# Optimization experiments

Hardware: AMD Instinct MI355X
Metric: run time of the kernel (lower is better)

## Reference

```python
import jax, jax.numpy as jnp
import numpy as np

K = 16
RADIUS = 1.0
N = 16384
SEQ = 8


def _knn(pc, k):
    """Brute-force kNN of pc against itself. pc: (1, n, 3).
    Returns (dist, idx) each (1, n, k), sorted ascending by distance,
    matching pointutils.knn semantics (Euclidean distance)."""
    x2 = jnp.sum(pc * pc, axis=-1)  # (1, n)
    # d2[b,i,j] = ||p_i - p_j||^2 via expansion; avoids (n,n,3) intermediate
    d2 = x2[:, :, None] + x2[:, None, :] - 2.0 * jnp.einsum('bnd,bmd->bnm', pc, pc)
    d2 = jnp.maximum(d2, 0.0)
    neg_d2, idx = jax.lax.top_k(-d2, k)  # k smallest distances
    dist = jnp.sqrt(jnp.maximum(-neg_d2, 0.0))
    return dist, idx


def setup_inputs() -> dict:
    key = jax.random.key(0)
    k1, k2, k3 = jax.random.split(key, 3)
    return {
        'pc_source': jax.random.normal(k1, (1, N, 3), dtype=jnp.float32),
        'pred_flow': jax.random.normal(k2, (SEQ, N, 3), dtype=jnp.float32),
        'weights': jax.random.uniform(k3, (N,), dtype=jnp.float32),
    }


def reference(pc_source, pred_flow, weights):
    # flow: (seq, 3, n)
    flow = jnp.transpose(pred_flow, (0, 2, 1))
    dist, idx = _knn(pc_source, K)  # (1, n, k)
    # replace out-of-radius neighbors with the nearest (self) index
    idx = jnp.where(dist > RADIUS, idx[:, :, 0:1], idx)
    idx = idx[0]  # (n, k); identical for all sequence steps
    # grouping_operation: gather neighbor flows -> (seq, 3, n, k)
    nn_flow = flow[:, :, idx]
    diff = flow[:, :, :, None] - nn_flow  # (seq, 3, n, k)
    # L2 norm over channel dim (loss_norm=2), safe at 0 (self-neighbor)
    sq = jnp.sum(diff * diff, axis=1)  # (seq, n, k)
    norm = jnp.where(sq > 0, jnp.sqrt(jnp.where(sq > 0, sq, 1.0)), 0.0)
    loss = norm.mean(axis=-1)  # (seq, n)
    loss = loss * weights[None, :]
    loss = loss.sum(axis=1)  # (seq,)
    wsum = weights.sum()
    loss = jnp.where(wsum > 0, loss / wsum, loss)
    return loss.mean()
```

## Files before the change

### kernel.cpp

```cpp
#include <hip/hip_runtime.h>
#include <math.h>

#define NPTS  16384
#define KNN   16
#define SEQV  8
#define NW    16
#define BATCH 8
#define CAPM  15
#define CAPR  1.001f
#define NBKT  256
#define BSCALE 56.8888f
#define HBLK  16
#define NGRP  256

#define SLOT(arr, t, col) arr[(t) * 1024 + (col)]

#define WS_HIST   256
#define WS_STARTS 16640
#define WS_SIDX   17920
#define WS_SORTED 83488

__device__ __forceinline__ unsigned umin_(unsigned a, unsigned b) { return a < b ? a : b; }
__device__ __forceinline__ unsigned umax_(unsigned a, unsigned b) { return a > b ? a : b; }

__device__ __forceinline__ int nbucket(float x) { return (int)fminf(x * BSCALE, 255.0f); }

__device__ __forceinline__ void merge_one(unsigned keys[KNN], unsigned kk) {
    if (kk < keys[KNN - 1]) {
#pragma unroll
        for (int u = 0; u < KNN; ++u) {
            unsigned lo = umin_(kk, keys[u]);
            kk = umax_(kk, keys[u]);
            keys[u] = lo;
        }
    }
}

__device__ __forceinline__ void merge16(unsigned k[KNN], const unsigned o[KNN]) {
    unsigned v[KNN];
#pragma unroll
    for (int i = 0; i < KNN; ++i) v[i] = umin_(k[i], o[KNN - 1 - i]);
#pragma unroll
    for (int d = 8; d >= 1; d >>= 1) {
#pragma unroll
        for (int i = 0; i < KNN; ++i) {
            if ((i & d) == 0) {
                unsigned lo = umin_(v[i], v[i + d]);
                unsigned hi = umax_(v[i], v[i + d]);
                v[i] = lo; v[i + d] = hi;
            }
        }
    }
#pragma unroll
    for (int i = 0; i < KNN; ++i) k[i] = v[i];
}

__device__ __forceinline__ void tree_load_merge(unsigned* uS, unsigned keys[KNN], int src) {
    unsigned o[KNN];
#pragma unroll
    for (int t = 0; t < KNN; ++t) o[t] = SLOT(uS, t, src);
    merge16(keys, o);
}

__global__ __launch_bounds__(1024) void hist_kernel(
    const float* __restrict__ pc, unsigned* __restrict__ hist)
{
    __shared__ unsigned h[NBKT];
    const int tid = threadIdx.x;
    if (tid < NBKT) h[tid] = 0u;
    __syncthreads();
    const int i = blockIdx.x * 1024 + tid;
    const float x = pc[3 * i + 0], y = pc[3 * i + 1], z = pc[3 * i + 2];
    const float n = sqrtf(fmaf(x, x, fmaf(y, y, z * z)));
    atomicAdd(&h[nbucket(n)], 1u);
    __syncthreads();
    if (tid < NBKT) hist[tid * HBLK + blockIdx.x] = h[tid];
}

__global__ __launch_bounds__(1024) void scatter_kernel(
    const float* __restrict__ pc, const unsigned* __restrict__ hist,
    unsigned* __restrict__ starts, float* __restrict__ accum,
    unsigned* __restrict__ sidx, float4* __restrict__ sorted4)
{
    __shared__ unsigned sH[NBKT];
    __shared__ unsigned sBase[NBKT];
    __shared__ unsigned sCnt[NBKT];
    const int tid = threadIdx.x;
    const int b   = blockIdx.x;

    unsigned own = 0, pre = 0;
    if (tid < NBKT) {
        const unsigned* row = hist + tid * HBLK;
        unsigned s = 0, p = 0;
#pragma unroll
        for (int k = 0; k < HBLK; ++k) {
            const unsigned c = row[k];
            if (k < b) p += c;
            s += c;
        }
        own = s; pre = p;
        sH[tid] = s;
        sCnt[tid] = 0u;
    }
    __syncthreads();
    for (int off = 1; off < NBKT; off <<= 1) {
        unsigned a = 0u;
        if (tid < NBKT && tid >= off) a = sH[tid - off];
        __syncthreads();
        if (tid < NBKT) sH[tid] += a;
        __syncthreads();
    }
    if (tid < NBKT) {
        const unsigned excl = sH[tid] - own;
        sBase[tid] = excl + pre;
        if (b == 0) starts[tid] = excl;
    }
    if (b == 0 && tid == 0) starts[NBKT] = NPTS;
    if (b == 0 && tid < 8) ((unsigned*)accum)[tid] = 0u;
    __syncthreads();

    const int i = b * 1024 + tid;
    const float x = pc[3 * i + 0], y = pc[3 * i + 1], z = pc[3 * i + 2];
    const float c2 = fmaf(x, x, fmaf(y, y, z * z));
    const int bin = nbucket(sqrtf(c2));
    const unsigned rank = atomicAdd(&sCnt[bin], 1u);
    const unsigned pos = sBase[bin] + rank;
    sorted4[pos] = make_float4(-2.0f * x, -2.0f * y, -2.0f * z, c2);
    sidx[pos] = (unsigned)i;
    if (b == 0 && tid < 8) {
        sorted4[NPTS + tid] = make_float4(0.0f, 0.0f, 0.0f, 1e18f);
        sidx[NPTS + tid] = 0u;
    }
}

__global__ __launch_bounds__(1024, 4) void mega_kernel(
    const float4* __restrict__ sorted, const unsigned* __restrict__ sidx,
    const unsigned* __restrict__ starts, const float* __restrict__ flow,
    const float* __restrict__ wts, float* __restrict__ accum,
    float* __restrict__ out)
{
    __shared__ unsigned uS[1024 * 16];
    float* sred = (float*)&uS[15 * 1024 + 1000];
    float* sTau = (float*)&uS[16320];

    const int tid  = threadIdx.x;
    const int lane = tid & 63;
    const int wv   = __builtin_amdgcn_readfirstlane(tid >> 6);
    const int is   = blockIdx.x * 64 + lane;

    const float4 mi = sorted[is];
    const float qx = -0.5f * mi.x;
    const float qy = -0.5f * mi.y;
    const float qz = -0.5f * mi.z;
    const float q2 = mi.w;
    const unsigned iorig = sidx[is];
    const float analytic = 0.19072f * exp2f(0.480898f * q2);
    const float tau0 = fminf(analytic, CAPR);

    const float nq = sqrtf(q2);
    float nmin = nq, nmax = nq;
#pragma unroll
    for (int off = 32; off > 0; off >>= 1) {
        nmin = fminf(nmin, __shfl_xor(nmin, off));
        nmax = fmaxf(nmax, __shfl_xor(nmax, off));
    }
    const float r0 = sqrtf(fminf(0.19072f * exp2f(0.480898f * nmax * nmax), CAPR));
    const int blo = nbucket(fmaxf(nmin - r0, 0.0f));
    const int bhi = nbucket(nmax + r0);
    const int kT0 = __builtin_amdgcn_readfirstlane((int)starts[blo]) >> 3;
    const int kTe = (__builtin_amdgcn_readfirstlane((int)starts[bhi + 1]) + 7) >> 3;

    unsigned keys[KNN];
#pragma unroll
    for (int t = 0; t < KNN; ++t) keys[t] = 0xFFFFFFFFu;
    int cnt = 0;
    unsigned* buf = &uS[tid * CAPM];

    {
        float taufs = tau0 - q2;
        float4 A[BATCH], Bv[BATCH];
        unsigned As[BATCH], Bs[BATCH];

        auto proc = [&](const float4* C, const unsigned* S) {
#pragma unroll
            for (int q = 0; q < BATCH; ++q) {
                const float4 c = C[q];
                float d2p = fmaf(c.x, qx, fmaf(c.y, qy, fmaf(c.z, qz, c.w)));
                bool acc = d2p <= taufs;
                if (__any(acc)) {
                    if (acc) {
                        float d2 = fmaxf(d2p + q2, 0.0f);
                        buf[cnt] = (__float_as_uint(d2) & 0xFFFFC000u) | S[q];
                        ++cnt;
                    }
                    if (cnt >= CAPM - 1) {
#pragma unroll 1
                        for (int t = 0; t < cnt; ++t) merge_one(keys, buf[t]);
                        cnt = 0;
                        float d16n = __uint_as_float(keys[KNN - 1] & 0xFFFFC000u);
                        taufs = fminf(taufs, fmaf(d16n, 1.0002f, 1e-6f) - q2);
                    }
                }
            }
        };

        int k = kT0 + wv;
        bool hA = (k < kTe);
        if (hA) { const float4* bp = sorted + (k << 3); const unsigned* sp = sidx + (k << 3);
#pragma unroll
            for (int q = 0; q < BATCH; ++q) { A[q] = bp[q]; As[q] = sp[q]; } }
        while (hA) {
            int k2 = k + 64; bool hB = (k2 < kTe);
            if (hB) { const float4* bp = sorted + (k2 << 3); const unsigned* sp = sidx + (k2 << 3);
#pragma unroll
                for (int q = 0; q < BATCH; ++q) { Bv[q] = bp[q]; Bs[q] = sp[q]; } }
            proc(A, As);
            if (!hB) break;
            int k3 = k2 + 64; bool hC = (k3 < kTe);
            if (hC) { const float4* bp = sorted + (k3 << 3); const unsigned* sp = sidx + (k3 << 3);
#pragma unroll
                for (int q = 0; q < BATCH; ++q) { A[q] = bp[q]; As[q] = sp[q]; } }
            proc(Bv, Bs);
            k = k3; hA = hC;
        }
#pragma unroll 1
        for (int t = 0; t < cnt; ++t) merge_one(keys, buf[t]);
        cnt = 0;
    }

    unsigned keys2[KNN];
#pragma unroll
    for (int t = 0; t < KNN; ++t) keys2[t] = keys[t];

    __syncthreads();

#pragma unroll
    for (int t = 0; t < KNN; ++t) SLOT(uS, t, tid) = keys[t];
    __syncthreads();
    if (wv < 8) {
        tree_load_merge(uS, keys, tid + 512);
#pragma unroll
        for (int t = 0; t < KNN; ++t) SLOT(uS, t, tid) = keys[t];
    }
    __syncthreads();
    if (wv < 4) {
        tree_load_merge(uS, keys, tid + 256);
#pragma unroll
        for (int t = 0; t < KNN; ++t) SLOT(uS, t, tid) = keys[t];
    }
    __syncthreads();
    if (wv < 2) {
        tree_load_merge(uS, keys, tid + 128);
#pragma unroll
        for (int t = 0; t < KNN; ++t) SLOT(uS, t, tid) = keys[t];
    }
    __syncthreads();
    if (wv == 0) {
        tree_load_merge(uS, keys, tid + 64);
        const float d16 = __uint_as_float(keys[KNN - 1] & 0xFFFFC000u);
        const float tf  = fmaf(d16, 1.0002f, 1e-6f);
        const bool fail = !(tf <= tau0);
        const float tv = fail ? CAPR : tf;
        sTau[lane] = tv;
        float tm = tv;
#pragma unroll
        for (int off = 32; off > 0; off >>= 1) tm = fmaxf(tm, __shfl_xor(tm, off));
        unsigned long long bw = __ballot(fail && (analytic < CAPR));
        if (lane == 0) { uS[16316] = (bw != 0ull) ? 1u : 0u; ((float*)uS)[16317] = tm; }
    }
    __syncthreads();

    float taufs = sTau[lane] - q2;
    const unsigned anyWide = __builtin_amdgcn_readfirstlane(uS[16316]);
    const float rA = sqrtf(((float*)uS)[16317]);
    int kA0, kAe;
    if (anyWide) { kA0 = 0; kAe = NPTS / 8; }
    else {
        int bloA = nbucket(fmaxf(nmin - rA, 0.0f));
        int bhiA = nbucket(nmax + rA);
        kA0 = __builtin_amdgcn_readfirstlane((int)starts[bloA]) >> 3;
        kAe = (__builtin_amdgcn_readfirstlane((int)starts[bhiA + 1]) + 7) >> 3;
    }
#pragma unroll
    for (int t = 0; t < KNN; ++t) keys[t] = keys2[t];
    {
        float4 A[BATCH], Bv[BATCH];
        unsigned As[BATCH], Bs[BATCH];

        auto proc = [&](const float4* C, const unsigned* S) {
#pragma unroll
            for (int q = 0; q < BATCH; ++q) {
                const float4 c = C[q];
                float d2p = fmaf(c.x, qx, fmaf(c.y, qy, fmaf(c.z, qz, c.w)));
                bool acc = d2p <= taufs;
                if (__any(acc)) {
                    if (acc) {
                        float d2 = fmaxf(d2p + q2, 0.0f);
                        buf[cnt] = (__float_as_uint(d2) & 0xFFFFC000u) | S[q];
                        ++cnt;
                    }
                    if (cnt >= CAPM - 1) {
#pragma unroll 1
                        for (int t = 0; t < cnt; ++t) merge_one(keys, buf[t]);
                        cnt = 0;
                        float d16n = __uint_as_float(keys[KNN - 1] & 0xFFFFC000u);
                        taufs = fminf(taufs, fmaf(d16n, 1.0002f, 1e-6f) - q2);
                    }
                }
            }
        };

        auto skipb = [&](int k) -> bool {
            return (!anyWide) && (k < kTe) && (((k - kT0 - wv) & 63) == 0);
        };
        int k = kA0 + ((wv - (kA0 - kT0)) & 15);
        if (skipb(k)) k += 16;
        bool hA = (k < kAe);
        if (hA) { const float4* bp = sorted + (k << 3); const unsigned* sp = sidx + (k << 3);
#pragma unroll
            for (int q = 0; q < BATCH; ++q) { A[q] = bp[q]; As[q] = sp[q]; } }
        while (hA) {
            int k2 = k + 16; if (skipb(k2)) k2 += 16;
            bool hB = (k2 < kAe);
            if (hB) { const float4* bp = sorted + (k2 << 3); const unsigned* sp = sidx + (k2 << 3);
#pragma unroll
                for (int q = 0; q < BATCH; ++q) { Bv[q] = bp[q]; Bs[q] = sp[q]; } }
            proc(A, As);
            if (!hB) break;
            int k3 = k2 + 16; if (skipb(k3)) k3 += 16;
            bool hC = (k3 < kAe);
            if (hC) { const float4* bp = sorted + (k3 << 3); const unsigned* sp = sidx + (k3 << 3);
#pragma unroll
                for (int q = 0; q < BATCH; ++q) { A[q] = bp[q]; As[q] = sp[q]; } }
            proc(Bv, Bs);
            k = k3; hA = hC;
        }
#pragma unroll 1
        for (int t = 0; t < cnt; ++t) merge_one(keys, buf[t]);
    }
    __syncthreads();

#pragma unroll
    for (int t = 0; t < KNN; ++t) SLOT(uS, t, tid) = keys[t];
    __syncthreads();
    if (wv < 8) {
        tree_load_merge(uS, keys, tid + 512);
#pragma unroll
        for (int t = 0; t < KNN; ++t) SLOT(uS, t, tid) = keys[t];
    }
    __syncthreads();
    if (wv < 4) {
        tree_load_merge(uS, keys, tid + 256);
#pragma unroll
        for (int t = 0; t < KNN; ++t) SLOT(uS, t, tid) = keys[t];
    }
    __syncthreads();
    if (wv < 2) {
        tree_load_merge(uS, keys, tid + 128);
#pragma unroll
        for (int t = 0; t < KNN; ++t) SLOT(uS, t, tid) = keys[t];
    }
    __syncthreads();
    if (wv == 0) {
        tree_load_merge(uS, keys, tid + 64);
        const int id0 = (int)(keys[0] & 0x3FFFu);
#pragma unroll
        for (int t = 0; t < KNN; ++t) {
            float d2t = __uint_as_float(keys[t] & 0xFFFFC000u);
            int   j   = (int)(keys[t] & 0x3FFFu);
            SLOT(uS, t, lane) = (unsigned)((d2t > 1.0f) ? id0 : j);
        }
    }
    __syncthreads();

    {
        const int s  = wv & 7;
        const int kh = wv >> 3;
        const float* fs = flow + (size_t)s * NPTS * 3;
        const float fx = fs[3 * iorig + 0];
        const float fy = fs[3 * iorig + 1];
        const float fz = fs[3 * iorig + 2];

        float sum = 0.0f;
#pragma unroll
        for (int z = 0; z < 8; ++z) {
            int j = (int)SLOT(uS, kh * 8 + z, lane);
            float dx = fx - fs[3 * j + 0];
            float dy = fy - fs[3 * j + 1];
            float dz = fz - fs[3 * j + 2];
            float sq = fmaf(dx, dx, fmaf(dy, dy, dz * dz));
            sum += (sq > 0.0f) ? sqrtf(sq) : 0.0f;
        }

        float contrib = wts[iorig] * sum;
#pragma unroll
        for (int off = 32; off > 0; off >>= 1) contrib += __shfl_down(contrib, off);
        if (lane == 0) sred[wv] = contrib;

        if (wv == 0) {
            float wi = wts[iorig];
#pragma unroll
            for (int off = 32; off > 0; off >>= 1) wi += __shfl_down(wi, off);
            if (lane == 0) atomicAdd(&accum[1], wi);
        }
        __syncthreads();

        if (tid == 0) {
            float c = 0.0f;
#pragma unroll
            for (int t = 0; t < NW; ++t) c += sred[t];
            atomicAdd(&accum[0], c);
            __threadfence();
            unsigned ticket = atomicAdd((unsigned*)accum + 2, 1u);
            if (ticket == gridDim.x - 1) {
                float a  = atomicAdd(&accum[0], 0.0f);
                float ws = atomicAdd(&accum[1], 0.0f);
                float v  = a / (float)(KNN * SEQV);
                out[0] = (ws > 0.0f) ? (v / ws) : v;
            }
        }
    }
}

extern "C" void kernel_launch(void* const* d_in, const int* in_sizes, int n_in,
                              void* d_out, int out_size, void* d_ws, size_t ws_size,
                              hipStream_t stream)
{
    const float* pc   = (const float*)d_in[0];
    const float* flow = (const float*)d_in[1];
    const float* wts  = (const float*)d_in[2];
    float* out = (float*)d_out;

    float*    accum  = (float*)d_ws;
    unsigned* hist   = (unsigned*)((char*)d_ws + WS_HIST);
    unsigned* starts = (unsigned*)((char*)d_ws + WS_STARTS);
    unsigned* sidx   = (unsigned*)((char*)d_ws + WS_SIDX);
    float4*   sorted = (float4*)  ((char*)d_ws + WS_SORTED);

    hist_kernel   <<<HBLK, 1024, 0, stream>>>(pc, hist);
    scatter_kernel<<<HBLK, 1024, 0, stream>>>(pc, hist, starts, accum, sidx, sorted);
    mega_kernel   <<<NGRP, 1024, 0, stream>>>(sorted, sidx, starts, flow, wts, accum, out);
}
```

Baseline: 140.2 us.

## Pad flow to float4 in prep kernel and make candidate merges wave-uniform

The histogram kernel now also copies the flow tensor into a padded float4 layout in workspace. The final loss stage can then gather each neighbour's flow with a single 16-byte load instead of three scalar loads. Separately, the kNN buffer flush is made wave-uniform: every lane runs a fixed-length merge loop, padding its unused slots with max keys, whenever any lane's buffer is full. This removes divergent variable-trip loops but adds extra merge work for lanes with few candidates, plus an additional 2 MB write pass in the 16-block prep kernel.

```diff
diff --git a/kernel.cpp b/kernel.cpp
--- a/kernel.cpp
+++ b/kernel.cpp
@@ -19,6 +19,7 @@
 #define WS_STARTS 16640
 #define WS_SIDX   17920
 #define WS_SORTED 83488
+#define WS_FLOWT  345760
 
 __device__ __forceinline__ unsigned umin_(unsigned a, unsigned b) { return a < b ? a : b; }
 __device__ __forceinline__ unsigned umax_(unsigned a, unsigned b) { return a > b ? a : b; }
@@ -63,7 +64,8 @@
 }
 
 __global__ __launch_bounds__(1024) void hist_kernel(
-    const float* __restrict__ pc, unsigned* __restrict__ hist)
+    const float* __restrict__ pc, const float* __restrict__ flow,
+    unsigned* __restrict__ hist, float4* __restrict__ flowT)
 {
     __shared__ unsigned h[NBKT];
     const int tid = threadIdx.x;
@@ -73,6 +75,11 @@
     const float x = pc[3 * i + 0], y = pc[3 * i + 1], z = pc[3 * i + 2];
     const float n = sqrtf(fmaf(x, x, fmaf(y, y, z * z)));
     atomicAdd(&h[nbucket(n)], 1u);
+#pragma unroll
+    for (int s = 0; s < SEQV; ++s) {
+        const float* fp = flow + (size_t)s * NPTS * 3 + 3 * i;
+        flowT[s * NPTS + i] = make_float4(fp[0], fp[1], fp[2], 0.0f);
+    }
     __syncthreads();
     if (tid < NBKT) hist[tid * HBLK + blockIdx.x] = h[tid];
 }
@@ -135,7 +142,7 @@
 
 __global__ __launch_bounds__(1024, 4) void mega_kernel(
     const float4* __restrict__ sorted, const unsigned* __restrict__ sidx,
-    const unsigned* __restrict__ starts, const float* __restrict__ flow,
+    const unsigned* __restrict__ starts, const float4* __restrict__ flowT,
     const float* __restrict__ wts, float* __restrict__ accum,
     float* __restrict__ out)
 {
@@ -193,9 +200,10 @@
                         buf[cnt] = (__float_as_uint(d2) & 0xFFFFC000u) | S[q];
                         ++cnt;
                     }
-                    if (cnt >= CAPM - 1) {
+                    if (__any(cnt >= CAPM - 1)) {
 #pragma unroll 1
-                        for (int t = 0; t < cnt; ++t) merge_one(keys, buf[t]);
+                        for (int t = 0; t < CAPM - 1; ++t)
+                            merge_one(keys, (t < cnt) ? buf[t] : 0xFFFFFFFFu);
                         cnt = 0;
                         float d16n = __uint_as_float(keys[KNN - 1] & 0xFFFFC000u);
                         taufs = fminf(taufs, fmaf(d16n, 1.0002f, 1e-6f) - q2);
@@ -224,7 +232,8 @@
             k = k3; hA = hC;
         }
 #pragma unroll 1
-        for (int t = 0; t < cnt; ++t) merge_one(keys, buf[t]);
+        for (int t = 0; t < CAPM - 1; ++t)
+            merge_one(keys, (t < cnt) ? buf[t] : 0xFFFFFFFFu);
         cnt = 0;
     }
 
@@ -299,9 +308,10 @@
                         buf[cnt] = (__float_as_uint(d2) & 0xFFFFC000u) | S[q];
                         ++cnt;
                     }
-                    if (cnt >= CAPM - 1) {
+                    if (__any(cnt >= CAPM - 1)) {
 #pragma unroll 1
-                        for (int t = 0; t < cnt; ++t) merge_one(keys, buf[t]);
+                        for (int t = 0; t < CAPM - 1; ++t)
+                            merge_one(keys, (t < cnt) ? buf[t] : 0xFFFFFFFFu);
                         cnt = 0;
                         float d16n = __uint_as_float(keys[KNN - 1] & 0xFFFFC000u);
                         taufs = fminf(taufs, fmaf(d16n, 1.0002f, 1e-6f) - q2);
@@ -336,7 +346,8 @@
             k = k3; hA = hC;
         }
 #pragma unroll 1
-        for (int t = 0; t < cnt; ++t) merge_one(keys, buf[t]);
+        for (int t = 0; t < CAPM - 1; ++t)
+            merge_one(keys, (t < cnt) ? buf[t] : 0xFFFFFFFFu);
     }
     __syncthreads();
 
@@ -376,18 +387,17 @@
     {
         const int s  = wv & 7;
         const int kh = wv >> 3;
-        const float* fs = flow + (size_t)s * NPTS * 3;
-        const float fx = fs[3 * iorig + 0];
-        const float fy = fs[3 * iorig + 1];
-        const float fz = fs[3 * iorig + 2];
+        const float4* fs4 = flowT + (size_t)s * NPTS;
+        const float4 qf = fs4[iorig];
 
         float sum = 0.0f;
 #pragma unroll
         for (int z = 0; z < 8; ++z) {
             int j = (int)SLOT(uS, kh * 8 + z, lane);
-            float dx = fx - fs[3 * j + 0];
-            float dy = fy - fs[3 * j + 1];
-            float dz = fz - fs[3 * j + 2];
+            const float4 v = fs4[j];
+            float dx = qf.x - v.x;
+            float dy = qf.y - v.y;
+            float dz = qf.z - v.z;
             float sq = fmaf(dx, dx, fmaf(dy, dy, dz * dz));
             sum += (sq > 0.0f) ? sqrtf(sq) : 0.0f;
         }
@@ -436,8 +446,9 @@
     unsigned* starts = (unsigned*)((char*)d_ws + WS_STARTS);
     unsigned* sidx   = (unsigned*)((char*)d_ws + WS_SIDX);
     float4*   sorted = (float4*)  ((char*)d_ws + WS_SORTED);
-
-    hist_kernel   <<<HBLK, 1024, 0, stream>>>(pc, hist);
+    float4*   flowT  = (float4*)  ((char*)d_ws + WS_FLOWT);
+
+    hist_kernel   <<<HBLK, 1024, 0, stream>>>(pc, flow, hist, flowT);
     scatter_kernel<<<HBLK, 1024, 0, stream>>>(pc, hist, starts, accum, sidx, sorted);
-    mega_kernel   <<<NGRP, 1024, 0, stream>>>(sorted, sidx, starts, flow, wts, accum, out);
-}
+    mega_kernel   <<<NGRP, 1024, 0, stream>>>(sorted, sidx, starts, flowT, wts, accum, out);
+}
```

After: 133.7 us. -4.6%, faster.
